# Kernel optimization log

Hardware: AMD Instinct MI355X
Metric: run time of the kernel (lower is better)

Reference implementation:

```python
import jax, jax.numpy as jnp
import numpy as np

EPS = 1e-4  # matches torch: x.norm(2, dim=1, keepdim=True) + 0.0001

def setup_inputs() -> dict:
    key = jax.random.key(0)
    k1, k2, k3 = jax.random.split(key, 3)
    B, IN, OUT = 16384, 2048, 2048
    x = jax.random.normal(k1, (B, IN), dtype=jnp.float32)
    # nn.Linear default init: U(-1/sqrt(in), 1/sqrt(in))
    bound = 1.0 / np.sqrt(IN)
    W = jax.random.uniform(k2, (OUT, IN), dtype=jnp.float32, minval=-bound, maxval=bound)
    b = jax.random.uniform(k3, (OUT,), dtype=jnp.float32, minval=-bound, maxval=bound)
    return {"x": x, "W": W, "b": b}

def reference(x, W, b):
    # L2-normalize each row, then Linear, then ReLU
    norm = jnp.linalg.norm(x, ord=2, axis=1, keepdims=True)  # [B, 1]
    x_dir = x / (norm + EPS)
    h = jnp.einsum('bi,oi->bo', x_dir, W) + b  # [B, OUT]
    return jax.nn.relu(h)
```

## Files before the change

kernel.cpp:

```cpp
#include <hip/hip_runtime.h>
#include <hip/hip_bf16.h>
#include <stdint.h>

#define B_ROWS 16384
#define IN_DIM 2048
#define OUT_DIM 2048

typedef __attribute__((ext_vector_type(4))) float f32x4;
typedef __attribute__((ext_vector_type(8))) short s16x8;

__device__ __forceinline__ unsigned short f2bf_rne(float f) {
  union { float f; unsigned u; } c; c.f = f;
  unsigned u = c.u;
  return (unsigned short)((u + 0x7FFFu + ((u >> 16) & 1u)) >> 16);
}

#define PREP_X_BLOCKS 4096
#define PREP_W_BLOCKS 2048

__global__ void __launch_bounds__(256) prep_kernel(const float* __restrict__ x,
                                                   unsigned short* __restrict__ xn,
                                                   float* __restrict__ scale,
                                                   const float* __restrict__ W,
                                                   unsigned short* __restrict__ Wb) {
  if (blockIdx.x < PREP_X_BLOCKS) {
    const int row  = (blockIdx.x * 256 + threadIdx.x) >> 6;
    const int lane = threadIdx.x & 63;
    const float4* xr = (const float4*)(x + (size_t)row * IN_DIM);
    unsigned short* xrow = xn + (size_t)row * IN_DIM;

    float ss = 0.0f;
    #pragma unroll
    for (int j = 0; j < 4; ++j) {
      const int f4 = j * 128 + lane * 2;
      float4 v0 = xr[f4 + 0];
      float4 v1 = xr[f4 + 1];
      ss += v0.x * v0.x + v0.y * v0.y + v0.z * v0.z + v0.w * v0.w +
            v1.x * v1.x + v1.y * v1.y + v1.z * v1.z + v1.w * v1.w;
      s16x8 p;
      p[0] = (short)f2bf_rne(v0.x); p[1] = (short)f2bf_rne(v0.y);
      p[2] = (short)f2bf_rne(v0.z); p[3] = (short)f2bf_rne(v0.w);
      p[4] = (short)f2bf_rne(v1.x); p[5] = (short)f2bf_rne(v1.y);
      p[6] = (short)f2bf_rne(v1.z); p[7] = (short)f2bf_rne(v1.w);
      *(s16x8*)(xrow + f4 * 4) = p;
    }

    #pragma unroll
    for (int m = 32; m > 0; m >>= 1) ss += __shfl_xor(ss, m, 64);
    if (lane == 0) scale[row] = 1.0f / (sqrtf(ss) + 1e-4f);
  } else {
    const size_t base = (size_t)(blockIdx.x - PREP_X_BLOCKS) * 2048 +
                        (size_t)threadIdx.x * 8;
    const float4* wp = (const float4*)(W + base);
    float4 v0 = wp[0];
    float4 v1 = wp[1];
    s16x8 p;
    p[0] = (short)f2bf_rne(v0.x); p[1] = (short)f2bf_rne(v0.y);
    p[2] = (short)f2bf_rne(v0.z); p[3] = (short)f2bf_rne(v0.w);
    p[4] = (short)f2bf_rne(v1.x); p[5] = (short)f2bf_rne(v1.y);
    p[6] = (short)f2bf_rne(v1.z); p[7] = (short)f2bf_rne(v1.w);
    *(s16x8*)(Wb + base) = p;
  }
}

__global__ void __launch_bounds__(256) gemm_kernel(const unsigned short* __restrict__ A,
                                                   const unsigned short* __restrict__ Bm,
                                                   const float* __restrict__ scale,
                                                   const float* __restrict__ bias,
                                                   float* __restrict__ out) {
  constexpr int BK = 64;
  __shared__ short As[128 * BK];
  __shared__ short Bs[128 * BK];

  const int tid = threadIdx.x;
  const int bid   = blockIdx.x;
  const int group = bid >> 7;
  const int w_    = bid & 127;
  const int bm    = group * 8 + (w_ & 7);
  const int bn    = w_ >> 3;

  const int lane = tid & 63;
  const int wave = tid >> 6;
  const int wm   = wave >> 1;
  const int wn   = wave & 1;
  const int lrow = lane & 15;
  const int lq   = lane >> 4;

  const int ar = tid >> 3;
  const int ac = ((tid & 7) ^ (ar & 7)) * 8;
  const unsigned short* ag = A  + (size_t)(bm * 128 + ar) * IN_DIM + ac;
  const unsigned short* bg = Bm + (size_t)(bn * 128 + ar) * IN_DIM + ac;
  char* asl = (char*)As + tid * 16;
  char* bsl = (char*)Bs + tid * 16;

  f32x4 acc[4][4] = {};

  for (int k0 = 0; k0 < IN_DIM; k0 += BK) {
    #pragma unroll
    for (int i = 0; i < 4; ++i) {
      __builtin_amdgcn_global_load_lds(
          (const __attribute__((address_space(1))) unsigned int*)(ag + (size_t)i * 32 * IN_DIM),
          (__attribute__((address_space(3))) unsigned int*)(asl + i * 4096), 16, 0, 0);
    }
    #pragma unroll
    for (int i = 0; i < 4; ++i) {
      __builtin_amdgcn_global_load_lds(
          (const __attribute__((address_space(1))) unsigned int*)(bg + (size_t)i * 32 * IN_DIM),
          (__attribute__((address_space(3))) unsigned int*)(bsl + i * 4096), 16, 0, 0);
    }
    ag += BK;
    bg += BK;
    __syncthreads();

    #pragma unroll
    for (int kk = 0; kk < 2; ++kk) {
      s16x8 af[4], bf[4];
      #pragma unroll
      for (int mi = 0; mi < 4; ++mi) {
        const int R = wm * 64 + mi * 16 + lrow;
        af[mi] = *(const s16x8*)(As + R * BK + (((kk * 4 + lq) ^ (lrow & 7)) * 8));
      }
      #pragma unroll
      for (int ni = 0; ni < 4; ++ni) {
        const int R = wn * 64 + ni * 16 + lrow;
        bf[ni] = *(const s16x8*)(Bs + R * BK + (((kk * 4 + lq) ^ (lrow & 7)) * 8));
      }
      #pragma unroll
      for (int mi = 0; mi < 4; ++mi)
        #pragma unroll
        for (int ni = 0; ni < 4; ++ni)
          acc[mi][ni] = __builtin_amdgcn_mfma_f32_16x16x32_bf16(af[mi], bf[ni], acc[mi][ni], 0, 0, 0);
    }
    __syncthreads();
  }

  const int row0 = bm * 128 + wm * 64 + lq * 4;
  const int col0 = bn * 128 + wn * 64 + lrow;
  #pragma unroll
  for (int mi = 0; mi < 4; ++mi) {
    const int row = row0 + mi * 16;
    const f32x4 sc = *(const f32x4*)(scale + row);
    #pragma unroll
    for (int ni = 0; ni < 4; ++ni) {
      const int col = col0 + ni * 16;
      const float bcol = bias[col];
      #pragma unroll
      for (int r = 0; r < 4; ++r) {
        float v = acc[mi][ni][r] * sc[r] + bcol;
        out[(size_t)(row + r) * OUT_DIM + col] = fmaxf(v, 0.0f);
      }
    }
  }
}

extern "C" void kernel_launch(void* const* d_in, const int* in_sizes, int n_in,
                              void* d_out, int out_size, void* d_ws, size_t ws_size,
                              hipStream_t stream) {
  const float* x = (const float*)d_in[0];
  const float* W = (const float*)d_in[1];
  const float* b = (const float*)d_in[2];
  float* out = (float*)d_out;

  char* ws = (char*)d_ws;
  unsigned short* xn    = (unsigned short*)ws;
  unsigned short* Wb    = (unsigned short*)(ws + (size_t)67108864);
  float*          scale = (float*)(ws + (size_t)67108864 + (size_t)8388608);

  prep_kernel<<<PREP_X_BLOCKS + PREP_W_BLOCKS, 256, 0, stream>>>(x, xn, scale, W, Wb);

  gemm_kernel<<<(OUT_DIM / 128) * (B_ROWS / 128), 256, 0, stream>>>(xn, Wb, scale, b, out);
}
```

Measured before the change: 372.4 us.

## Register-prefetch next K tile in GEMM instead of direct global-to-LDS loads

Replaces the direct global_load_lds copies with a register-staged software pipeline. The next K tile is loaded into registers while the current tile is written to LDS and consumed by the MFMAs. The syncthreads calls become raw barriers, and only lgkmcnt is waited on so the global prefetch stays in flight across the compute. This aims to hide global memory latency. In exchange it uses more VGPRs and adds explicit LDS store instructions, and the manual waitcnt encoding is fragile.

```diff
diff --git a/kernel.cpp b/kernel.cpp
--- a/kernel.cpp
+++ b/kernel.cpp
@@ -69,6 +69,7 @@
                                                    const float* __restrict__ bias,
                                                    float* __restrict__ out) {
   constexpr int BK = 64;
+  constexpr int NITER = IN_DIM / BK;
   __shared__ short As[128 * BK];
   __shared__ short Bs[128 * BK];
 
@@ -94,23 +95,36 @@
   char* bsl = (char*)Bs + tid * 16;
 
   f32x4 acc[4][4] = {};
+  s16x8 a_st[4], b_st[4];
 
-  for (int k0 = 0; k0 < IN_DIM; k0 += BK) {
+  #pragma unroll
+  for (int i = 0; i < 4; ++i) {
+    a_st[i] = *(const s16x8*)(ag + (size_t)i * 32 * IN_DIM);
+    b_st[i] = *(const s16x8*)(bg + (size_t)i * 32 * IN_DIM);
+  }
+  ag += BK;
+  bg += BK;
+
+  for (int k0 = 0; k0 < NITER; ++k0) {
     #pragma unroll
     for (int i = 0; i < 4; ++i) {
-      __builtin_amdgcn_global_load_lds(
-          (const __attribute__((address_space(1))) unsigned int*)(ag + (size_t)i * 32 * IN_DIM),
-          (__attribute__((address_space(3))) unsigned int*)(asl + i * 4096), 16, 0, 0);
+      *(s16x8*)(asl + i * 4096) = a_st[i];
+      *(s16x8*)(bsl + i * 4096) = b_st[i];
     }
-    #pragma unroll
-    for (int i = 0; i < 4; ++i) {
-      __builtin_amdgcn_global_load_lds(
-          (const __attribute__((address_space(1))) unsigned int*)(bg + (size_t)i * 32 * IN_DIM),
-          (__attribute__((address_space(3))) unsigned int*)(bsl + i * 4096), 16, 0, 0);
+    if (k0 + 1 < NITER) {
+      #pragma unroll
+      for (int i = 0; i < 4; ++i) {
+        a_st[i] = *(const s16x8*)(ag + (size_t)i * 32 * IN_DIM);
+        b_st[i] = *(const s16x8*)(bg + (size_t)i * 32 * IN_DIM);
+      }
+      ag += BK;
+      bg += BK;
     }
-    ag += BK;
-    bg += BK;
-    __syncthreads();
+
+    asm volatile("" ::: "memory");
+    __builtin_amdgcn_s_waitcnt(0xC07F);
+    __builtin_amdgcn_s_barrier();
+    asm volatile("" ::: "memory");
 
     #pragma unroll
     for (int kk = 0; kk < 2; ++kk) {
@@ -131,7 +145,10 @@
         for (int ni = 0; ni < 4; ++ni)
           acc[mi][ni] = __builtin_amdgcn_mfma_f32_16x16x32_bf16(af[mi], bf[ni], acc[mi][ni], 0, 0, 0);
     }
-    __syncthreads();
+
+    asm volatile("" ::: "memory");
+    __builtin_amdgcn_s_barrier();
+    asm volatile("" ::: "memory");
   }
 
   const int row0 = bm * 128 + wm * 64 + lq * 4;
```

Result: slower. 395.4 us (+6.2%).
